# Kernel tuning notes

Measured on AMD Instinct MI355X. Metric: run time of the kernel, lower is better.

Reference implementation:

```python
import jax, jax.numpy as jnp
import numpy as np

N = 8192
EPS = 1e-7  # matches torch BCE's internal log clamping behavior


def setup_inputs() -> dict:
    key = jax.random.key(0)
    ks = jax.random.split(key, 8)
    return {
        "solar_score": jax.random.normal(ks[0], (N,), dtype=jnp.float32),
        "solar_ranking_gt": jax.random.randint(ks[1], (N,), 0, 1000000, dtype=jnp.int64),
        "capacity_pred": jax.random.normal(ks[2], (N,), dtype=jnp.float32),
        "capacity_gt": jax.random.normal(ks[3], (N,), dtype=jnp.float32),
        "roi_pred": jax.random.normal(ks[4], (N,), dtype=jnp.float32),
        "roi_gt": jax.random.normal(ks[5], (N,), dtype=jnp.float32),
        "viable_pred": jax.random.uniform(ks[6], (N,), dtype=jnp.float32, minval=1e-4, maxval=1.0 - 1e-4),
        "viable_gt": jax.random.uniform(ks[7], (N,), dtype=jnp.float32),
    }


def _pairwise_ranking_loss(scores, gt_ranking):
    n = scores.shape[0]
    # pair (i, j) with i < j contributes iff gt_ranking[i] < gt_ranking[j]
    upper = jnp.triu(jnp.ones((n, n), dtype=bool), k=1)
    mask = (gt_ranking[:, None] < gt_ranking[None, :]) & upper
    hinge = jax.nn.relu(1.0 - (scores[:, None] - scores[None, :]))  # [n, n]
    count = jnp.sum(mask)
    total = jnp.sum(jnp.where(mask, hinge, 0.0))
    return jnp.where(count > 0, total / count.astype(scores.dtype), jnp.zeros((), scores.dtype))


def reference(solar_score, solar_ranking_gt, capacity_pred, capacity_gt,
              roi_pred, roi_gt, viable_pred, viable_gt):
    ranking_loss = _pairwise_ranking_loss(solar_score, solar_ranking_gt)

    capacity_loss = jnp.mean((capacity_pred - capacity_gt) ** 2)

    d = roi_pred - roi_gt  # smooth_l1 with beta=1 (torch default)
    ad = jnp.abs(d)
    roi_loss = jnp.mean(jnp.where(ad < 1.0, 0.5 * d * d, ad - 0.5))

    p = jnp.clip(viable_pred, EPS, 1.0 - EPS)
    viability_loss = -jnp.mean(viable_gt * jnp.log(p) + (1.0 - viable_gt) * jnp.log1p(-p))

    return (ranking_loss + capacity_loss + roi_loss + viability_loss) / 4.0
```

## Files before the change

kernel.cpp:

```cpp
#include <hip/hip_runtime.h>

#define NELEM 8192
#define H 4
#define NSTRIP (NELEM / H)
#define NPAIR (NSTRIP / 2)
#define NTHREADS 512
#define JTILE (NTHREADS * 4)
#define EPSV 1e-7f
#define MAGIC32 0xA5C3F17Du

__global__ __launch_bounds__(NTHREADS, 4) void solar_fused_kernel(
    const float* __restrict__ s, const int* __restrict__ r,
    const float* __restrict__ cp, const float* __restrict__ cg,
    const float* __restrict__ rp, const float* __restrict__ rg,
    const float* __restrict__ vp, const float* __restrict__ vg,
    unsigned long long* __restrict__ pw, float* __restrict__ out) {

    const int b   = blockIdx.x;
    const int tid = threadIdx.x;

    __shared__ float  rf[NTHREADS / 64][3];
    __shared__ double dd[NTHREADS / 64][2];
    __shared__ float  fe[NTHREADS / 64];

    if (b == NPAIR) {
        const int i0 = tid;
        const int i1 = tid + NTHREADS;

        unsigned long long w1a = __hip_atomic_load(&pw[2 * i0 + 1], __ATOMIC_RELAXED, __HIP_MEMORY_SCOPE_AGENT);
        unsigned long long w1b = __hip_atomic_load(&pw[2 * i1 + 1], __ATOMIC_RELAXED, __HIP_MEMORY_SCOPE_AGENT);
        while ((unsigned)(w1a >> 32) != MAGIC32) {
            __builtin_amdgcn_s_sleep(2);
            w1a = __hip_atomic_load(&pw[2 * i0 + 1], __ATOMIC_RELAXED, __HIP_MEMORY_SCOPE_AGENT);
        }
        while ((unsigned)(w1b >> 32) != MAGIC32) {
            __builtin_amdgcn_s_sleep(2);
            w1b = __hip_atomic_load(&pw[2 * i1 + 1], __ATOMIC_RELAXED, __HIP_MEMORY_SCOPE_AGENT);
        }
        const unsigned long long w0a = __hip_atomic_load(&pw[2 * i0], __ATOMIC_RELAXED, __HIP_MEMORY_SCOPE_AGENT);
        const unsigned long long w0b = __hip_atomic_load(&pw[2 * i1], __ATOMIC_RELAXED, __HIP_MEMORY_SCOPE_AGENT);

        double tsum = (double)__uint_as_float((unsigned)w0a) + (double)__uint_as_float((unsigned)w0b);
        double cnt  = (double)__uint_as_float((unsigned)(w0a >> 32)) + (double)__uint_as_float((unsigned)(w0b >> 32));
        float  ext  = __uint_as_float((unsigned)w1a) + __uint_as_float((unsigned)w1b);

#pragma unroll
        for (int off = 32; off > 0; off >>= 1) {
            tsum += __shfl_down(tsum, off);
            cnt  += __shfl_down(cnt,  off);
            ext  += __shfl_down(ext,  off);
        }

        const int wave = tid >> 6;
        const int lane = tid & 63;
        if (lane == 0) { dd[wave][0] = tsum; dd[wave][1] = cnt; fe[wave] = ext; }
        __syncthreads();

        if (tid == 0) {
            double t = 0.0, cn = 0.0;
            float e = 0.0f;
#pragma unroll
            for (int w = 0; w < NTHREADS / 64; ++w) { t += dd[w][0]; cn += dd[w][1]; e += fe[w]; }
            const float rank = (cn > 0.0) ? (float)(t / cn) : 0.0f;
            out[0] = 0.25f * rank + e * (0.25f / (float)NELEM);
        }
        return;
    }

    const int joff = tid * 4;
    const int i0a = 4 * b;
    const int i0b = 8188 - 4 * b;

    const float4 sa4 = *reinterpret_cast<const float4*>(s + i0a);
    const int4   ra4 = *reinterpret_cast<const int4*>(r + i0a);
    const float4 sb4 = *reinterpret_cast<const float4*>(s + i0b);
    const int4   rb4 = *reinterpret_cast<const int4*>(r + i0b);
    const float4 c1a = make_float4(1.0f - sa4.x, 1.0f - sa4.y, 1.0f - sa4.z, 1.0f - sa4.w);
    const float4 c1b = make_float4(1.0f - sb4.x, 1.0f - sb4.y, 1.0f - sb4.z, 1.0f - sb4.w);

    float tacc[4] = {0.0f, 0.0f, 0.0f, 0.0f};
    int   cacc[4] = {0, 0, 0, 0};

    auto comp_full = [&](float4 sj, int4 rj, float4 c1, int4 ri) {
        const float c1e[4] = {c1.x, c1.y, c1.z, c1.w};
        const int   rie[4] = {ri.x, ri.y, ri.z, ri.w};
        const float sje[4] = {sj.x, sj.y, sj.z, sj.w};
        const int   rje[4] = {rj.x, rj.y, rj.z, rj.w};
#pragma unroll
        for (int k = 0; k < 4; ++k) {
#pragma unroll
            for (int e = 0; e < 4; ++e) {
                const bool cond = rie[k] < rje[e];
                const float h = fmaxf(0.0f, c1e[k] + sje[e]);
                tacc[e] += cond ? h : 0.0f;
                cacc[e] += cond ? 1 : 0;
            }
        }
    };

    auto comp_diag = [&](float4 sj, int4 rj, float4 c1, int4 ri, int jb, int i0) {
        const float c1e[4] = {c1.x, c1.y, c1.z, c1.w};
        const int   rie[4] = {ri.x, ri.y, ri.z, ri.w};
        const float sje[4] = {sj.x, sj.y, sj.z, sj.w};
        const int   rje[4] = {rj.x, rj.y, rj.z, rj.w};
#pragma unroll
        for (int k = 0; k < 4; ++k) {
#pragma unroll
            for (int e = 0; e < 4; ++e) {
                const bool cond = ((jb + e) > (i0 + k)) & (rie[k] < rje[e]);
                const float h = fmaxf(0.0f, c1e[k] + sje[e]);
                tacc[e] += cond ? h : 0.0f;
                cacc[e] += cond ? 1 : 0;
            }
        }
    };

    if (b < 512) {
        const int jb0 = joff, jb1 = JTILE + joff, jb2 = 2 * JTILE + joff, jb3 = 3 * JTILE + joff;
        const float4 s0 = *reinterpret_cast<const float4*>(s + jb0);
        const float4 s1 = *reinterpret_cast<const float4*>(s + jb1);
        const float4 s2 = *reinterpret_cast<const float4*>(s + jb2);
        const float4 s3 = *reinterpret_cast<const float4*>(s + jb3);
        const int4   r0 = *reinterpret_cast<const int4*>(r + jb0);
        const int4   r1 = *reinterpret_cast<const int4*>(r + jb1);
        const int4   r2 = *reinterpret_cast<const int4*>(r + jb2);
        const int4   r3 = *reinterpret_cast<const int4*>(r + jb3);

        comp_diag(s0, r0, c1a, ra4, jb0, i0a);
        comp_full(s1, r1, c1a, ra4);
        comp_full(s2, r2, c1a, ra4);
        comp_full(s3, r3, c1a, ra4);
        comp_diag(s3, r3, c1b, rb4, jb3, i0b);
    } else {
        const int jb1 = JTILE + joff, jb2 = 2 * JTILE + joff, jb3 = 3 * JTILE + joff;
        const float4 s1 = *reinterpret_cast<const float4*>(s + jb1);
        const float4 s2 = *reinterpret_cast<const float4*>(s + jb2);
        const float4 s3 = *reinterpret_cast<const float4*>(s + jb3);
        const int4   r1 = *reinterpret_cast<const int4*>(r + jb1);
        const int4   r2 = *reinterpret_cast<const int4*>(r + jb2);
        const int4   r3 = *reinterpret_cast<const int4*>(r + jb3);

        comp_diag(s1, r1, c1a, ra4, jb1, i0a);
        comp_full(s2, r2, c1a, ra4);
        comp_full(s3, r3, c1a, ra4);
        comp_diag(s2, r2, c1b, rb4, jb2, i0b);
        comp_full(s3, r3, c1b, rb4);
    }

    float ext = 0.0f;
    if (tid < 8) {
        const int i = b * 8 + tid;
        const float dc = cp[i] - cg[i];
        const float cap = dc * dc;
        const float dr = rp[i] - rg[i];
        const float ad = fabsf(dr);
        const float roi = (ad < 1.0f) ? 0.5f * dr * dr : (ad - 0.5f);
        const float p = fminf(fmaxf(vp[i], EPSV), 1.0f - EPSV);
        const float g = vg[i];
        const float bce = g * logf(p) + (1.0f - g) * log1pf(-p);
        ext = cap + roi - bce;
    }

    float tsum = (tacc[0] + tacc[1]) + (tacc[2] + tacc[3]);
    int   cnti = (cacc[0] + cacc[1]) + (cacc[2] + cacc[3]);

#pragma unroll
    for (int off = 32; off > 0; off >>= 1) {
        tsum += __shfl_down(tsum, off);
        cnti += __shfl_down(cnti, off);
        ext  += __shfl_down(ext,  off);
    }

    const int wave = tid >> 6;
    const int lane = tid & 63;
    if (lane == 0) { rf[wave][0] = tsum; rf[wave][1] = (float)cnti; rf[wave][2] = ext; }
    __syncthreads();

    if (tid == 0) {
        float bt = 0.0f, bc = 0.0f, be = 0.0f;
#pragma unroll
        for (int w = 0; w < NTHREADS / 64; ++w) {
            bt += rf[w][0]; bc += rf[w][1]; be += rf[w][2];
        }
        const unsigned long long w0 =
            ((unsigned long long)__float_as_uint(bc) << 32) | (unsigned long long)__float_as_uint(bt);
        const unsigned long long w1 =
            ((unsigned long long)MAGIC32 << 32) | (unsigned long long)__float_as_uint(be);
        __hip_atomic_store(&pw[2 * b], w0, __ATOMIC_RELAXED, __HIP_MEMORY_SCOPE_AGENT);
        asm volatile("s_waitcnt vmcnt(0)" ::: "memory");
        __hip_atomic_store(&pw[2 * b + 1], w1, __ATOMIC_RELAXED, __HIP_MEMORY_SCOPE_AGENT);
    }
}

extern "C" void kernel_launch(void* const* d_in, const int* in_sizes, int n_in,
                              void* d_out, int out_size, void* d_ws, size_t ws_size,
                              hipStream_t stream) {
    const float* s  = (const float*)d_in[0];
    const int*   r  = (const int*)d_in[1];
    const float* cp = (const float*)d_in[2];
    const float* cg = (const float*)d_in[3];
    const float* rp = (const float*)d_in[4];
    const float* rg = (const float*)d_in[5];
    const float* vp = (const float*)d_in[6];
    const float* vg = (const float*)d_in[7];
    float* out = (float*)d_out;
    unsigned long long* pw = (unsigned long long*)d_ws;

    solar_fused_kernel<<<NPAIR + 1, NTHREADS, 0, stream>>>(s, r, cp, cg, rp, rg, vp, vg, pw, out);
}
```

Measured before the change: 12.98 us.

## Fold final reduction into block 0, ballot-count pairs, skip empty diagonal tiles

Removes the dedicated reducer block: block 0 finishes its own tile, then spins on every block's tagged partials and writes the output. Pair counts are now taken per wave with ballot and popcount instead of per-lane integer accumulators. Diagonal tiles are skipped when no lane in the wave needs them, and their loads are deferred until then. The count is packed into 16 bits with a tag, so both words carry a tag and the wait between the two stores is dropped. In exchange, per-block counts must fit in 16 bits, and the spin-wait needs all 1024 blocks to be co-resident.

```diff
diff --git a/kernel.cpp b/kernel.cpp
--- a/kernel.cpp
+++ b/kernel.cpp
@@ -1,12 +1,11 @@
 #include <hip/hip_runtime.h>
 
 #define NELEM 8192
-#define H 4
-#define NSTRIP (NELEM / H)
-#define NPAIR (NSTRIP / 2)
+#define NPAIR 1024
 #define NTHREADS 512
 #define JTILE (NTHREADS * 4)
 #define EPSV 1e-7f
+#define TAG16   0xA5C3u
 #define MAGIC32 0xA5C3F17Du
 
 __global__ __launch_bounds__(NTHREADS, 4) void solar_fused_kernel(
@@ -19,53 +18,12 @@
     const int b   = blockIdx.x;
     const int tid = threadIdx.x;
 
-    __shared__ float  rf[NTHREADS / 64][3];
-    __shared__ double dd[NTHREADS / 64][2];
-    __shared__ float  fe[NTHREADS / 64];
-
-    if (b == NPAIR) {
-        const int i0 = tid;
-        const int i1 = tid + NTHREADS;
-
-        unsigned long long w1a = __hip_atomic_load(&pw[2 * i0 + 1], __ATOMIC_RELAXED, __HIP_MEMORY_SCOPE_AGENT);
-        unsigned long long w1b = __hip_atomic_load(&pw[2 * i1 + 1], __ATOMIC_RELAXED, __HIP_MEMORY_SCOPE_AGENT);
-        while ((unsigned)(w1a >> 32) != MAGIC32) {
-            __builtin_amdgcn_s_sleep(2);
-            w1a = __hip_atomic_load(&pw[2 * i0 + 1], __ATOMIC_RELAXED, __HIP_MEMORY_SCOPE_AGENT);
-        }
-        while ((unsigned)(w1b >> 32) != MAGIC32) {
-            __builtin_amdgcn_s_sleep(2);
-            w1b = __hip_atomic_load(&pw[2 * i1 + 1], __ATOMIC_RELAXED, __HIP_MEMORY_SCOPE_AGENT);
-        }
-        const unsigned long long w0a = __hip_atomic_load(&pw[2 * i0], __ATOMIC_RELAXED, __HIP_MEMORY_SCOPE_AGENT);
-        const unsigned long long w0b = __hip_atomic_load(&pw[2 * i1], __ATOMIC_RELAXED, __HIP_MEMORY_SCOPE_AGENT);
-
-        double tsum = (double)__uint_as_float((unsigned)w0a) + (double)__uint_as_float((unsigned)w0b);
-        double cnt  = (double)__uint_as_float((unsigned)(w0a >> 32)) + (double)__uint_as_float((unsigned)(w0b >> 32));
-        float  ext  = __uint_as_float((unsigned)w1a) + __uint_as_float((unsigned)w1b);
-
-#pragma unroll
-        for (int off = 32; off > 0; off >>= 1) {
-            tsum += __shfl_down(tsum, off);
-            cnt  += __shfl_down(cnt,  off);
-            ext  += __shfl_down(ext,  off);
-        }
-
-        const int wave = tid >> 6;
-        const int lane = tid & 63;
-        if (lane == 0) { dd[wave][0] = tsum; dd[wave][1] = cnt; fe[wave] = ext; }
-        __syncthreads();
-
-        if (tid == 0) {
-            double t = 0.0, cn = 0.0;
-            float e = 0.0f;
-#pragma unroll
-            for (int w = 0; w < NTHREADS / 64; ++w) { t += dd[w][0]; cn += dd[w][1]; e += fe[w]; }
-            const float rank = (cn > 0.0) ? (float)(t / cn) : 0.0f;
-            out[0] = 0.25f * rank + e * (0.25f / (float)NELEM);
-        }
-        return;
-    }
+    __shared__ float    rft[NTHREADS / 64];
+    __shared__ float    rfe[NTHREADS / 64];
+    __shared__ unsigned rcu[NTHREADS / 64];
+    __shared__ double   dd[NTHREADS / 64];
+    __shared__ unsigned cc[NTHREADS / 64];
+    __shared__ float    fe[NTHREADS / 64];
 
     const int joff = tid * 4;
     const int i0a = 4 * b;
@@ -78,8 +36,8 @@
     const float4 c1a = make_float4(1.0f - sa4.x, 1.0f - sa4.y, 1.0f - sa4.z, 1.0f - sa4.w);
     const float4 c1b = make_float4(1.0f - sb4.x, 1.0f - sb4.y, 1.0f - sb4.z, 1.0f - sb4.w);
 
-    float tacc[4] = {0.0f, 0.0f, 0.0f, 0.0f};
-    int   cacc[4] = {0, 0, 0, 0};
+    float    tacc[4] = {0.0f, 0.0f, 0.0f, 0.0f};
+    unsigned cnt_u   = 0;
 
     auto comp_full = [&](float4 sj, int4 rj, float4 c1, int4 ri) {
         const float c1e[4] = {c1.x, c1.y, c1.z, c1.w};
@@ -93,7 +51,7 @@
                 const bool cond = rie[k] < rje[e];
                 const float h = fmaxf(0.0f, c1e[k] + sje[e]);
                 tacc[e] += cond ? h : 0.0f;
-                cacc[e] += cond ? 1 : 0;
+                cnt_u += (unsigned)__popcll(__ballot(cond));
             }
         }
     };
@@ -110,29 +68,13 @@
                 const bool cond = ((jb + e) > (i0 + k)) & (rie[k] < rje[e]);
                 const float h = fmaxf(0.0f, c1e[k] + sje[e]);
                 tacc[e] += cond ? h : 0.0f;
-                cacc[e] += cond ? 1 : 0;
+                cnt_u += (unsigned)__popcll(__ballot(cond));
             }
         }
     };
 
     if (b < 512) {
         const int jb0 = joff, jb1 = JTILE + joff, jb2 = 2 * JTILE + joff, jb3 = 3 * JTILE + joff;
-        const float4 s0 = *reinterpret_cast<const float4*>(s + jb0);
-        const float4 s1 = *reinterpret_cast<const float4*>(s + jb1);
-        const float4 s2 = *reinterpret_cast<const float4*>(s + jb2);
-        const float4 s3 = *reinterpret_cast<const float4*>(s + jb3);
-        const int4   r0 = *reinterpret_cast<const int4*>(r + jb0);
-        const int4   r1 = *reinterpret_cast<const int4*>(r + jb1);
-        const int4   r2 = *reinterpret_cast<const int4*>(r + jb2);
-        const int4   r3 = *reinterpret_cast<const int4*>(r + jb3);
-
-        comp_diag(s0, r0, c1a, ra4, jb0, i0a);
-        comp_full(s1, r1, c1a, ra4);
-        comp_full(s2, r2, c1a, ra4);
-        comp_full(s3, r3, c1a, ra4);
-        comp_diag(s3, r3, c1b, rb4, jb3, i0b);
-    } else {
-        const int jb1 = JTILE + joff, jb2 = 2 * JTILE + joff, jb3 = 3 * JTILE + joff;
         const float4 s1 = *reinterpret_cast<const float4*>(s + jb1);
         const float4 s2 = *reinterpret_cast<const float4*>(s + jb2);
         const float4 s3 = *reinterpret_cast<const float4*>(s + jb3);
@@ -140,11 +82,37 @@
         const int4   r2 = *reinterpret_cast<const int4*>(r + jb2);
         const int4   r3 = *reinterpret_cast<const int4*>(r + jb3);
 
-        comp_diag(s1, r1, c1a, ra4, jb1, i0a);
+        comp_full(s1, r1, c1a, ra4);
         comp_full(s2, r2, c1a, ra4);
         comp_full(s3, r3, c1a, ra4);
-        comp_diag(s2, r2, c1b, rb4, jb2, i0b);
+
+        if (__any((jb0 + 3) > i0a)) {
+            const float4 s0 = *reinterpret_cast<const float4*>(s + jb0);
+            const int4   r0 = *reinterpret_cast<const int4*>(r + jb0);
+            comp_diag(s0, r0, c1a, ra4, jb0, i0a);
+        }
+        if (__any((jb3 + 3) > i0b)) {
+            comp_diag(s3, r3, c1b, rb4, jb3, i0b);
+        }
+    } else {
+        const int jb1 = JTILE + joff, jb2 = 2 * JTILE + joff, jb3 = 3 * JTILE + joff;
+        const float4 s2 = *reinterpret_cast<const float4*>(s + jb2);
+        const float4 s3 = *reinterpret_cast<const float4*>(s + jb3);
+        const int4   r2 = *reinterpret_cast<const int4*>(r + jb2);
+        const int4   r3 = *reinterpret_cast<const int4*>(r + jb3);
+
+        comp_full(s2, r2, c1a, ra4);
+        comp_full(s3, r3, c1a, ra4);
         comp_full(s3, r3, c1b, rb4);
+
+        if (__any((jb1 + 3) > i0a)) {
+            const float4 s1 = *reinterpret_cast<const float4*>(s + jb1);
+            const int4   r1 = *reinterpret_cast<const int4*>(r + jb1);
+            comp_diag(s1, r1, c1a, ra4, jb1, i0a);
+        }
+        if (__any((jb2 + 3) > i0b)) {
+            comp_diag(s2, r2, c1b, rb4, jb2, i0b);
+        }
     }
 
     float ext = 0.0f;
@@ -162,33 +130,70 @@
     }
 
     float tsum = (tacc[0] + tacc[1]) + (tacc[2] + tacc[3]);
-    int   cnti = (cacc[0] + cacc[1]) + (cacc[2] + cacc[3]);
-
 #pragma unroll
     for (int off = 32; off > 0; off >>= 1) {
         tsum += __shfl_down(tsum, off);
-        cnti += __shfl_down(cnti, off);
         ext  += __shfl_down(ext,  off);
     }
 
     const int wave = tid >> 6;
     const int lane = tid & 63;
-    if (lane == 0) { rf[wave][0] = tsum; rf[wave][1] = (float)cnti; rf[wave][2] = ext; }
+    if (lane == 0) { rft[wave] = tsum; rfe[wave] = ext; rcu[wave] = cnt_u; }
     __syncthreads();
 
     if (tid == 0) {
-        float bt = 0.0f, bc = 0.0f, be = 0.0f;
-#pragma unroll
-        for (int w = 0; w < NTHREADS / 64; ++w) {
-            bt += rf[w][0]; bc += rf[w][1]; be += rf[w][2];
-        }
+        float bt = 0.0f, be = 0.0f;
+        unsigned bc = 0;
+#pragma unroll
+        for (int w = 0; w < NTHREADS / 64; ++w) { bt += rft[w]; be += rfe[w]; bc += rcu[w]; }
         const unsigned long long w0 =
-            ((unsigned long long)__float_as_uint(bc) << 32) | (unsigned long long)__float_as_uint(bt);
+            ((unsigned long long)((TAG16 << 16) | (bc & 0xFFFFu)) << 32) | (unsigned long long)__float_as_uint(bt);
         const unsigned long long w1 =
             ((unsigned long long)MAGIC32 << 32) | (unsigned long long)__float_as_uint(be);
-        __hip_atomic_store(&pw[2 * b], w0, __ATOMIC_RELAXED, __HIP_MEMORY_SCOPE_AGENT);
-        asm volatile("s_waitcnt vmcnt(0)" ::: "memory");
+        __hip_atomic_store(&pw[2 * b],     w0, __ATOMIC_RELAXED, __HIP_MEMORY_SCOPE_AGENT);
         __hip_atomic_store(&pw[2 * b + 1], w1, __ATOMIC_RELAXED, __HIP_MEMORY_SCOPE_AGENT);
+    }
+
+    if (b == 0) {
+        double   td = 0.0;
+        unsigned cn = 0;
+        float    ex = 0.0f;
+#pragma unroll
+        for (int q = 0; q < 2; ++q) {
+            const int blk = tid + q * NTHREADS;
+            unsigned long long w0 = __hip_atomic_load(&pw[2 * blk], __ATOMIC_RELAXED, __HIP_MEMORY_SCOPE_AGENT);
+            while ((unsigned)(w0 >> 48) != TAG16) {
+                __builtin_amdgcn_s_sleep(2);
+                w0 = __hip_atomic_load(&pw[2 * blk], __ATOMIC_RELAXED, __HIP_MEMORY_SCOPE_AGENT);
+            }
+            unsigned long long w1 = __hip_atomic_load(&pw[2 * blk + 1], __ATOMIC_RELAXED, __HIP_MEMORY_SCOPE_AGENT);
+            while ((unsigned)(w1 >> 32) != MAGIC32) {
+                __builtin_amdgcn_s_sleep(2);
+                w1 = __hip_atomic_load(&pw[2 * blk + 1], __ATOMIC_RELAXED, __HIP_MEMORY_SCOPE_AGENT);
+            }
+            td += (double)__uint_as_float((unsigned)w0);
+            cn += (unsigned)((w0 >> 32) & 0xFFFFu);
+            ex += __uint_as_float((unsigned)w1);
+        }
+
+#pragma unroll
+        for (int off = 32; off > 0; off >>= 1) {
+            td += __shfl_down(td, off);
+            cn += __shfl_down(cn, off);
+            ex += __shfl_down(ex, off);
+        }
+        if (lane == 0) { dd[wave] = td; cc[wave] = cn; fe[wave] = ex; }
+        __syncthreads();
+
+        if (tid == 0) {
+            double t = 0.0;
+            unsigned long long c = 0;
+            float e = 0.0f;
+#pragma unroll
+            for (int w = 0; w < NTHREADS / 64; ++w) { t += dd[w]; c += cc[w]; e += fe[w]; }
+            const float rank = (c > 0) ? (float)(t / (double)c) : 0.0f;
+            out[0] = 0.25f * rank + e * (0.25f / (float)NELEM);
+        }
     }
 }
 
@@ -206,5 +211,5 @@
     float* out = (float*)d_out;
     unsigned long long* pw = (unsigned long long*)d_ws;
 
-    solar_fused_kernel<<<NPAIR + 1, NTHREADS, 0, stream>>>(s, r, cp, cg, rp, rg, vp, vg, pw, out);
+    solar_fused_kernel<<<NPAIR, NTHREADS, 0, stream>>>(s, r, cp, cg, rp, rg, vp, vg, pw, out);
 }
```

Result: faster. 12.19 us (-6.1%).
